# Performance work log

Hardware: AMD Instinct MI355X
Metric: run time of the kernel (lower is better)

## Reference

```python
import jax, jax.numpy as jnp
import numpy as np
from jax import lax

B, T, DIN = 512, 96, 64
H = 256          # hidden_dim
P = 2            # patch_size
L = 4            # n_layers
HEADS = 8
E = 3 * H        # encoder_dim = hidden_dim * len(scales)
NC = 100         # num_classes
EPS = 1e-5


def layernorm(x, g, b):
    m = x.mean(-1, keepdims=True)
    v = ((x - m) ** 2).mean(-1, keepdims=True)
    return (x - m) * lax.rsqrt(v + EPS) * g + b


def conv1d(x, w, b, k):
    # x: [B, C, T], w: [O, I, k]; torch padding='same' (extra pad on the right for even k)
    lo = (k - 1) // 2
    hi = (k - 1) - lo
    y = lax.conv_general_dilated(x, w, (1,), [(lo, hi)],
                                 dimension_numbers=('NCH', 'OIH', 'NCH'))
    return y + b[None, :, None]


def fourier_attn(x, Wqkv, Wo, bo):
    Bx, Tx, Ex = x.shape
    dh = Ex // HEADS
    qkv = x @ Wqkv                                   # [B,T,3E]
    q, k, v = jnp.split(qkv, 3, axis=-1)
    to_heads = lambda t: t.reshape(Bx, Tx, HEADS, dh).transpose(0, 2, 1, 3)  # [B,h,T,dh]
    q, k, v = to_heads(q), to_heads(k), to_heads(v)
    qf = jnp.fft.rfft(q, axis=-2)
    kf = jnp.fft.rfft(k, axis=-2)
    attn = jnp.sum(jnp.conj(qf) * kf, axis=-1).real * (dh ** -0.5)  # [B,h,F]
    attn = jax.nn.softmax(attn, axis=-1)
    vf = jnp.fft.rfft(v, axis=-2)                    # [B,h,F,dh]
    out = jnp.fft.irfft(attn[..., None] * vf, n=Tx, axis=-2)        # [B,h,T,dh]
    out = out.transpose(0, 2, 1, 3).reshape(Bx, Tx, Ex)
    return out @ Wo + bo


def setup_inputs() -> dict:
    key = jax.random.key(0)
    ks = iter(jax.random.split(key, 40))
    nrm = lambda shape, s=0.02: jax.random.normal(next(ks), shape, jnp.float32) * s
    z = lambda *shape: jnp.zeros(shape, jnp.float32)
    o = lambda *shape: jnp.ones(shape, jnp.float32)
    return dict(
        x=jax.random.normal(next(ks), (B, T, DIN), jnp.float32),
        W_in=nrm((DIN, H)), b_in=z(H),
        pe=nrm((1, 100, H)),
        W_shape=nrm((H, H)), b_shape=z(H),
        W_patch=nrm((P * H, H)), b_patch=z(H),
        conv_w1=nrm((H, H, 1)), conv_b1=z(H),
        conv_w2=nrm((H, H, 2)), conv_b2=z(H),
        conv_w4=nrm((H, H, 4)), conv_b4=z(H),
        ln1_g=o(L, E), ln1_b=z(L, E),
        Wqkv=nrm((L, E, 3 * E)),
        Wo=nrm((L, E, E)), bo=z(L, E),
        ln2_g=o(L, E), ln2_b=z(L, E),
        Wf1=nrm((L, E, 4 * E)), bf1=z(L, 4 * E),
        Wf2=nrm((L, 4 * E, E)), bf2=z(L, E),
        ssm_w=nrm((E, E, 3)), ssm_b=z(E),
        ssm_g=o(E), ssm_bn=z(E),
        W_out=nrm((E, NC)), b_out=z(NC),
    )


def reference(x, W_in, b_in, pe, W_shape, b_shape, W_patch, b_patch,
              conv_w1, conv_b1, conv_w2, conv_b2, conv_w4, conv_b4,
              ln1_g, ln1_b, Wqkv, Wo, bo, ln2_g, ln2_b, Wf1, bf1, Wf2, bf2,
              ssm_w, ssm_b, ssm_g, ssm_bn, W_out, b_out):
    h = x @ W_in + b_in                              # [B,T,H]
    h = h + pe[:, :h.shape[1], :]
    # shape-aware embedding: diff with prepend of first step
    sf = jnp.diff(h, axis=1, prepend=h[:, :1, :])
    h = h + sf @ W_shape + b_shape
    # patch embedding: [B,T,H] -> [B,T/P,P*H] -> [B,T/P,H]
    Bx, Tx, Dx = h.shape
    h = h.reshape(Bx, Tx // P, P * Dx) @ W_patch + b_patch
    # multiscale fourier: rfft.real then 3 same-padded convs, concat channels
    f = jnp.fft.rfft(h, axis=1).real                 # [B,F,H], F = T/P//2 + 1
    fc = f.transpose(0, 2, 1)                        # [B,H,F]
    m1 = conv1d(fc, conv_w1, conv_b1, 1).transpose(0, 2, 1)
    m2 = conv1d(fc, conv_w2, conv_b2, 2).transpose(0, 2, 1)
    m4 = conv1d(fc, conv_w4, conv_b4, 4).transpose(0, 2, 1)
    h = jnp.concatenate([m1, m2, m4], axis=-1)       # [B,F,E]
    for i in range(L):
        h = h + fourier_attn(layernorm(h, ln1_g[i], ln1_b[i]), Wqkv[i], Wo[i], bo[i])
        y = layernorm(h, ln2_g[i], ln2_b[i])
        y = jax.nn.gelu(y @ Wf1[i] + bf1[i], approximate=False) @ Wf2[i] + bf2[i]
        h = h + y
    # simple SSM: depth conv residual + layernorm
    s = conv1d(h.transpose(0, 2, 1), ssm_w, ssm_b, 3).transpose(0, 2, 1)
    h = layernorm(h + s, ssm_g, ssm_bn)
    return h.mean(axis=1) @ W_out + b_out            # [B,NC]
```

## Files before the change

kernel.cpp:

```cpp
#include <hip/hip_runtime.h>
#include <hip/hip_bf16.h>
#include <math.h>

#define Bsz 512
#define Tin 96
#define DIN 64
#define Hd  256
#define Pp  2
#define Ll  4
#define NHEAD 8
#define Ed  768
#define NCls 100
#define Tp  48
#define Ff  25
#define F2  13
#define DH  96

#define E_BIAS 1
#define E_PE   2
#define E_RES  4
#define E_ACC  8
#define E_GELU 16
#define E_OUTS 32
#define E_SPLK 64

typedef unsigned short ushortT;
typedef unsigned short ushort8 __attribute__((ext_vector_type(8)));
typedef short short8 __attribute__((ext_vector_type(8)));
typedef float f32x4 __attribute__((ext_vector_type(4)));

static __device__ __forceinline__ ushortT f2bf(float f) {
  __hip_bfloat16 h = __float2bfloat16(f);
  return *reinterpret_cast<ushortT*>(&h);
}
static __device__ __forceinline__ float bfbits2f(ushortT u) {
  unsigned int x = ((unsigned int)u) << 16;
  return __uint_as_float(x);
}
static __device__ __forceinline__ void split2(float v, ushortT& h, ushortT& l) {
  h = f2bf(v);
  l = f2bf(v - bfbits2f(h));
}

typedef const __attribute__((address_space(1))) void* gas1_t;
typedef __attribute__((address_space(3))) void* las3_t;
static __device__ __forceinline__ void gload16(const void* g, void* l) {
  __builtin_amdgcn_global_load_lds((gas1_t)g, (las3_t)l, 16, 0, 0);
}

constexpr int GBN = 128, GBK = 32;

template<int BMS, int AMODE, int ASRC, int EPI>
__global__ __launch_bounds__(256) void gemm3(
    const float* __restrict__ A,
    const ushortT* __restrict__ Ah, const ushortT* __restrict__ Al,
    const ushortT* __restrict__ Bh, const ushortT* __restrict__ Bl,
    const float* __restrict__ bias, const float* __restrict__ extra,
    float* __restrict__ C, ushortT* __restrict__ Coh, ushortT* __restrict__ Col,
    int M, int N, int K, int Ald, int Tdim, int lo, int Kin, int Cld, int coff,
    int Mt, int Nt, int mmaj, int ksn)
{
  constexpr int GBMv = BMS;
  constexpr int WMF  = GBMv / 32;
  constexpr int ARPW = GBMv / 4;
  constexpr int TPR  = 256 / GBMv;
  constexpr int EPT  = 32 / TPR;

  __shared__ __align__(16) ushortT Ash[GBMv * GBK];
  __shared__ __align__(16) ushortT Asl[GBMv * GBK];
  __shared__ __align__(16) ushortT Bsh[GBN * GBK];
  __shared__ __align__(16) ushortT Bsl[GBN * GBK];
  int tid = threadIdx.x;

  int lin = blockIdx.x;
  int G = gridDim.x;
  int r8 = lin & 7, s8 = lin >> 3;
  int q = G >> 3, rem = G & 7;
  int start = r8 * q + (r8 < rem ? r8 : rem);
  int idx = start + s8;
  int tiles = Mt * Nt;
  int ks = 0;
  if (ksn > 1) { ks = idx / tiles; idx -= ks * tiles; }
  int mt, nt;
  if (mmaj) { mt = idx / Nt; nt = idx - mt * Nt; }
  else      { nt = idx / Mt; mt = idx - nt * Mt; }
  int m0 = mt * GBMv, n0 = nt * GBN;
  int kper = K / ksn;
  int kbeg = ks * kper, kend = kbeg + kper;

  int wid = tid >> 6, lane = tid & 63;
  int wm = wid & 1, wn = wid >> 1;
  int m16 = lane & 15, quad = lane >> 4;

  f32x4 acc[WMF][4] = {};

  int gcb = (lane & 3) << 4;
  int growB = (wid << 5) + (lane >> 2);
  int scbB  = gcb ^ (((growB >> 1) & 3) << 4);
  char* ldsB = (char*)Bsh + (wid << 11);
  char* ldsb = (char*)Bsl + (wid << 11);
  size_t bo0 = ((size_t)(n0 + growB) * K) * 2 + scbB;
  size_t bo1 = bo0 + (size_t)16 * K * 2;
  int growA = wid * ARPW + (lane >> 2);
  int scbA  = gcb ^ (((growA >> 1) & 3) << 4);
  char* ldsA = (char*)Ash + wid * ARPW * 64;
  char* ldsa = (char*)Asl + wid * ARPW * 64;
  size_t ao0 = 0, ao1 = 0;
  if (ASRC == 1) {
    int ar0 = m0 + growA;  if (ar0 >= M) ar0 = M - 1;
    ao0 = ((size_t)ar0 * Ald) * 2 + scbA;
    if (ARPW == 32) {
      int ar1 = m0 + growA + 16;  if (ar1 >= M) ar1 = M - 1;
      ao1 = ((size_t)ar1 * Ald) * 2 + scbA;
    }
  }

  int srow = tid / TPR;
  int sseg = (tid % TPR) * EPT;
  int sswz = ((srow >> 1) & 3) << 3;

  int fswz = ((m16 >> 1) & 3) << 3;
  int scf  = (quad << 3) ^ fswz;

  for (int k0 = kbeg; k0 < kend; k0 += GBK) {
    size_t kb = (size_t)k0 * 2;
    gload16((const char*)Bh + bo0 + kb, ldsB);
    gload16((const char*)Bh + bo1 + kb, ldsB + 1024);
    gload16((const char*)Bl + bo0 + kb, ldsb);
    gload16((const char*)Bl + bo1 + kb, ldsb + 1024);
    if (ASRC == 1) {
      gload16((const char*)Ah + ao0 + kb, ldsA);
      gload16((const char*)Al + ao0 + kb, ldsa);
      if (ARPW == 32) {
        gload16((const char*)Ah + ao1 + kb, ldsA + 1024);
        gload16((const char*)Al + ao1 + kb, ldsa + 1024);
      }
    } else {
      int row = m0 + srow;
      if (row >= M) row = M - 1;
      float tf[EPT];
      if (AMODE == 0) {
        const float* p = A + (size_t)row * Ald + k0 + sseg;
#pragma unroll
        for (int j = 0; j < EPT; j += 4) {
          float4 v = *(const float4*)(p + j);
          tf[j] = v.x; tf[j+1] = v.y; tf[j+2] = v.z; tf[j+3] = v.w;
        }
      } else if (AMODE == 1) {
        int t = row % Tdim;
        const float* p = A + (size_t)row * Ald + k0 + sseg;
#pragma unroll
        for (int j = 0; j < EPT; j += 4) {
          float4 v = *(const float4*)(p + j);
          float4 w = (t != 0) ? *(const float4*)(p - Ald + j) : v;
          tf[j] = v.x - w.x; tf[j+1] = v.y - w.y;
          tf[j+2] = v.z - w.z; tf[j+3] = v.w - w.w;
        }
      } else {
        int kk = k0 + sseg;
        int tap = kk / Kin;
        int i0  = kk - tap * Kin;
        int bb = row / Tdim;
        int t  = row - bb * Tdim;
        int tt = t - lo + tap;
        if (tt >= 0 && tt < Tdim) {
          const float* p = A + ((size_t)bb * Tdim + tt) * Ald + i0;
#pragma unroll
          for (int j = 0; j < EPT; j += 4) {
            float4 v = *(const float4*)(p + j);
            tf[j] = v.x; tf[j+1] = v.y; tf[j+2] = v.z; tf[j+3] = v.w;
          }
        } else {
#pragma unroll
          for (int j = 0; j < EPT; j++) tf[j] = 0.0f;
        }
      }
      ushortT th[EPT], tl[EPT];
#pragma unroll
      for (int j = 0; j < EPT; j++) split2(tf[j], th[j], tl[j]);
#pragma unroll
      for (int c8 = 0; c8 < EPT / 8; c8++) {
        int st = srow * GBK + ((sseg + c8 * 8) ^ sswz);
        *(ushort8*)&Ash[st] = *(ushort8*)&th[c8 * 8];
        *(ushort8*)&Asl[st] = *(ushort8*)&tl[c8 * 8];
      }
    }
    __syncthreads();
    short8 ah[WMF], al[WMF], bh[4], bl[4];
#pragma unroll
    for (int i = 0; i < WMF; i++) {
      int ro = (wm * (WMF * 16) + i * 16 + m16) * GBK + scf;
      ah[i] = *(short8*)&Ash[ro];
      al[i] = *(short8*)&Asl[ro];
    }
#pragma unroll
    for (int j = 0; j < 4; j++) {
      int ro = (wn * 64 + j * 16 + m16) * GBK + scf;
      bh[j] = *(short8*)&Bsh[ro];
      bl[j] = *(short8*)&Bsl[ro];
    }
    __builtin_amdgcn_s_setprio(1);
#pragma unroll
    for (int i = 0; i < WMF; i++)
#pragma unroll
      for (int j = 0; j < 4; j++) {
        acc[i][j] = __builtin_amdgcn_mfma_f32_16x16x32_bf16(ah[i], bh[j], acc[i][j], 0, 0, 0);
        acc[i][j] = __builtin_amdgcn_mfma_f32_16x16x32_bf16(al[i], bh[j], acc[i][j], 0, 0, 0);
        acc[i][j] = __builtin_amdgcn_mfma_f32_16x16x32_bf16(ah[i], bl[j], acc[i][j], 0, 0, 0);
      }
    __builtin_amdgcn_s_setprio(0);
    __syncthreads();
  }

#pragma unroll
  for (int i = 0; i < WMF; i++) {
#pragma unroll
    for (int j = 0; j < 4; j++) {
      int colg = n0 + wn * 64 + j * 16 + m16;
#pragma unroll
      for (int rr = 0; rr < 4; rr++) {
        int rowg = m0 + wm * (WMF * 16) + i * 16 + quad * 4 + rr;
        if (rowg >= M) continue;
        float v = acc[i][j][rr];
        if ((EPI & E_BIAS) && ks == 0) v += bias[colg];
        if (EPI & E_PE)   v += extra[(size_t)(rowg % Tdim) * N + colg];
        if (EPI & E_RES)  v += extra[(size_t)rowg * Cld + colg];
        if (EPI & E_GELU) v = 0.5f * v * (1.0f + erff(v * 0.70710678118654752f));
        size_t off = (size_t)rowg * Cld + coff + colg;
        if (EPI & E_SPLK) {
          atomicAdd(&C[off], v);
        } else if (EPI & E_OUTS) {
          ushortT h, l; split2(v, h, l);
          Coh[off] = h; Col[off] = l;
        } else {
          if (EPI & E_ACC) v += C[off];
          C[off] = v;
        }
      }
    }
  }
}

#define GEMM3(BMS_, AM, AS, EP, KS, Asrc, AhP, AlP, BhP, BlP, biasP, extraP, CP, CohP, ColP, \
              Mv, Nv, Kv, AldV, TdimV, loV, KinV, CldV, coffV) \
  do { int Mt_ = ((Mv) + (BMS_) - 1) / (BMS_), Nt_ = (Nv) / GBN; \
       int mm_ = ((Mv) >= (Nv)) ? 1 : 0; \
       gemm3<BMS_, AM, AS, EP><<<dim3(Mt_ * Nt_ * (KS)), dim3(256), 0, stream>>>( \
           Asrc, AhP, AlP, BhP, BlP, biasP, extraP, CP, CohP, ColP, \
           Mv, Nv, Kv, AldV, TdimV, loV, KinV, CldV, coffV, Mt_, Nt_, mm_, KS); } while (0)

__global__ __launch_bounds__(256) void wcvt_t_split(
    const float* __restrict__ W, ushortT* __restrict__ Wh, ushortT* __restrict__ Wl,
    int K, int N)
{
  __shared__ float t[32][33];
  int k0 = blockIdx.y * 32, n0 = blockIdx.x * 32;
  int tx = threadIdx.x;
  int ty = threadIdx.y;
#pragma unroll
  for (int dy = 0; dy < 32; dy += 8)
    t[ty + dy][tx] = W[(size_t)(k0 + ty + dy) * N + n0 + tx];
  __syncthreads();
#pragma unroll
  for (int dy = 0; dy < 32; dy += 8) {
    float v = t[tx][ty + dy];
    ushortT h, l;
    split2(v, h, l);
    size_t off = (size_t)(n0 + ty + dy) * K + k0 + tx;
    Wh[off] = h; Wl[off] = l;
  }
}

__global__ __launch_bounds__(256) void wcvt_split(
    const float* __restrict__ W, ushortT* __restrict__ Wh, ushortT* __restrict__ Wl, int n)
{
  int gid = blockIdx.x * 256 + threadIdx.x;
  int stride = gridDim.x * 256;
  for (int i = gid; i < n; i += stride) {
    ushortT h, l;
    split2(W[i], h, l);
    Wh[i] = h; Wl[i] = l;
  }
}

__global__ __launch_bounds__(256) void wcvt_split_tm(
    const float* __restrict__ W, ushortT* __restrict__ Wh, ushortT* __restrict__ Wl,
    int O, int Kin, int NT)
{
  int n = O * Kin * NT;
  int gid = blockIdx.x * 256 + threadIdx.x;
  int stride = gridDim.x * 256;
  for (int idx = gid; idx < n; idx += stride) {
    int o = idx / (Kin * NT);
    int rr = idx - o * (Kin * NT);
    int tap = rr / Kin;
    int i = rr - tap * Kin;
    float v = W[(size_t)o * Kin * NT + (size_t)i * NT + tap];
    ushortT h, l;
    split2(v, h, l);
    Wh[idx] = h; Wl[idx] = l;
  }
}

constexpr int BM = 64, BN = 64, BK = 16, TM = 4, TN = 4;
__global__ __launch_bounds__(256) void gemm_cls(
    const float* __restrict__ A, const float* __restrict__ Bw,
    const float* __restrict__ bias, float* __restrict__ C,
    int M, int N, int K, int Ald, int Cld)
{
  __shared__ alignas(16) float As[BK][BM + 4];
  __shared__ alignas(16) float Bs[BK][BN + 4];
  int tid = threadIdx.x;
  int n0 = blockIdx.x * BN;
  int m0 = blockIdx.y * BM;
  int tx = tid & 15, ty = tid >> 4;
  float acc[TM][TN];
#pragma unroll
  for (int i = 0; i < TM; i++)
#pragma unroll
    for (int j = 0; j < TN; j++) acc[i][j] = 0.0f;
  int a_m = tid >> 2, a_k = (tid & 3) * 4;
  int b_k = tid >> 4, b_n = (tid & 15) * 4;
  for (int k0 = 0; k0 < K; k0 += BK) {
    int row = m0 + a_m;
#pragma unroll
    for (int j = 0; j < 4; j++)
      As[a_k + j][a_m] = A[(size_t)row * Ald + k0 + a_k + j];
    int kk = k0 + b_k;
#pragma unroll
    for (int j = 0; j < 4; j++) {
      int nn = n0 + b_n + j;
      Bs[b_k][b_n + j] = (nn < N) ? Bw[(size_t)kk * N + nn] : 0.0f;
    }
    __syncthreads();
#pragma unroll
    for (int k = 0; k < BK; k++) {
      float4 av = *reinterpret_cast<const float4*>(&As[k][ty * TM]);
      float4 bv = *reinterpret_cast<const float4*>(&Bs[k][tx * TN]);
      float a4[4] = {av.x, av.y, av.z, av.w};
      float b4[4] = {bv.x, bv.y, bv.z, bv.w};
#pragma unroll
      for (int i = 0; i < TM; i++)
#pragma unroll
        for (int j = 0; j < TN; j++) acc[i][j] += a4[i] * b4[j];
    }
    __syncthreads();
  }
#pragma unroll
  for (int i = 0; i < TM; i++) {
    int row = m0 + ty * TM + i;
#pragma unroll
    for (int j = 0; j < TN; j++) {
      int col = n0 + tx * TN + j;
      if (col >= N) continue;
      C[(size_t)row * Cld + col] = acc[i][j] + bias[col];
    }
  }
}

__global__ __launch_bounds__(256) void rfft48_kernel(
    const float* __restrict__ hp, float* __restrict__ f)
{
  int kf = blockIdx.x;
  int b  = blockIdx.y;
  int tid = threadIdx.x;
  __shared__ float ct[48];
  if (tid < 48) {
    int rr = (kf * tid) % 48;
    ct[tid] = cosf(6.2831853071795864f * (float)rr / 48.0f);
  }
  __syncthreads();
  const float* hb = hp + (size_t)b * Tp * Hd;
  float s = 0.0f;
  for (int t = 0; t < 48; t++) s += hb[t * Hd + tid] * ct[t];
  f[((size_t)b * Ff + kf) * Hd + tid] = s;
}

__global__ __launch_bounds__(256) void attn_fused(
    const float* __restrict__ qkv,
    ushortT* __restrict__ oh, ushortT* __restrict__ ol)
{
  int bh = blockIdx.x;
  int b = bh >> 3, h = bh & 7;
  __shared__ float qs[Ff * DH], ks[Ff * DH], vs[Ff * DH];
  __shared__ float ct[F2 * Ff], st[F2 * Ff];
  __shared__ float red[F2 * DH];
  __shared__ float sm[F2];
  __shared__ float G[Ff];
  int tid = threadIdx.x;
  const float* base = qkv + (size_t)b * Ff * (3 * Ed) + h * DH;
  for (int e = tid; e < Ff * DH; e += 256) {
    int t = e / DH, d = e - t * DH;
    size_t ro = (size_t)t * (3 * Ed) + d;
    qs[e] = base[ro];
    ks[e] = base[ro + Ed];
    vs[e] = base[ro + 2 * Ed];
  }
  for (int e = tid; e < F2 * Ff; e += 256) {
    int fq = e / Ff, t = e - fq * Ff;
    int rr = (fq * t) % Ff;
    float ang = 6.2831853071795864f * (float)rr / 25.0f;
    ct[e] = cosf(ang); st[e] = sinf(ang);
  }
  __syncthreads();
  for (int e = tid; e < F2 * DH; e += 256) {
    int fq = e / DH, d = e - fq * DH;
    float qr = 0, qi = 0, kr = 0, ki = 0;
    for (int t = 0; t < Ff; t++) {
      float c = ct[fq * Ff + t], s = st[fq * Ff + t];
      float qv = qs[t * DH + d], kv = ks[t * DH + d];
      qr += qv * c; qi += qv * s; kr += kv * c; ki += kv * s;
    }
    red[e] = qr * kr + qi * ki;
  }
  __syncthreads();
  if (tid < F2) {
    float s = 0;
    for (int d = 0; d < DH; d++) s += red[tid * DH + d];
    sm[tid] = s * 0.10206207261596575f;
  }
  __syncthreads();
  if (tid == 0) {
    float mx = sm[0];
    for (int f = 1; f < F2; f++) mx = fmaxf(mx, sm[f]);
    float den = 0;
    for (int f = 0; f < F2; f++) { float e2 = expf(sm[f] - mx); sm[f] = e2; den += e2; }
    float inv = 1.0f / den;
    for (int f = 0; f < F2; f++)
      sm[f] *= inv * ((f == 0) ? (1.0f / 25.0f) : (2.0f / 25.0f));
  }
  __syncthreads();
  if (tid < Ff) {
    float g = 0;
    for (int f = 0; f < F2; f++) g += sm[f] * ct[f * Ff + tid];
    G[tid] = g;
  }
  __syncthreads();
  size_t ob = ((size_t)b * Ff) * Ed + h * DH;
  for (int e = tid; e < Ff * DH; e += 256) {
    int t = e / DH, d = e - t * DH;
    float o = 0;
    int dd = t;
    for (int tp = 0; tp < Ff; tp++) {
      o += G[dd] * vs[tp * DH + d];
      dd--; if (dd < 0) dd += Ff;
    }
    ushortT hh, ll;
    split2(o, hh, ll);
    size_t off = ob + (size_t)t * Ed + d;
    oh[off] = hh; ol[off] = ll;
  }
}

static __device__ __forceinline__ float wave_sum(float s) {
#pragma unroll
  for (int o = 32; o > 0; o >>= 1) s += __shfl_xor(s, o);
  return s;
}

__global__ __launch_bounds__(256) void ln_split(
    const float* __restrict__ x, const float* __restrict__ g,
    const float* __restrict__ bb, ushortT* __restrict__ yh, ushortT* __restrict__ yl)
{
  int row = blockIdx.x;
  int tid = threadIdx.x;
  int wid = tid >> 6, lane = tid & 63;
  const float* xr = x + (size_t)row * Ed;
  float v0 = xr[tid], v1 = xr[tid + 256], v2 = xr[tid + 512];
  __shared__ float wsum[4], wsq[4];
  float s = wave_sum(v0 + v1 + v2);
  if (lane == 0) wsum[wid] = s;
  __syncthreads();
  float m = (wsum[0] + wsum[1] + wsum[2] + wsum[3]) * (1.0f / 768.0f);
  float d0 = v0 - m, d1 = v1 - m, d2 = v2 - m;
  float q = wave_sum(d0 * d0 + d1 * d1 + d2 * d2);
  if (lane == 0) wsq[wid] = q;
  __syncthreads();
  float inv = rsqrtf((wsq[0] + wsq[1] + wsq[2] + wsq[3]) * (1.0f / 768.0f) + 1e-5f);
  size_t basei = (size_t)row * Ed;
  float o0 = d0 * inv * g[tid] + bb[tid];
  float o1 = d1 * inv * g[tid + 256] + bb[tid + 256];
  float o2 = d2 * inv * g[tid + 512] + bb[tid + 512];
  ushortT h, l;
  split2(o0, h, l); yh[basei + tid] = h;       yl[basei + tid] = l;
  split2(o1, h, l); yh[basei + tid + 256] = h; yl[basei + tid + 256] = l;
  split2(o2, h, l); yh[basei + tid + 512] = h; yl[basei + tid + 512] = l;
}

__global__ __launch_bounds__(256) void ln_f32(
    const float* __restrict__ x, const float* __restrict__ g,
    const float* __restrict__ bb, float* __restrict__ y)
{
  int row = blockIdx.x;
  int tid = threadIdx.x;
  int wid = tid >> 6, lane = tid & 63;
  const float* xr = x + (size_t)row * Ed;
  float v0 = xr[tid], v1 = xr[tid + 256], v2 = xr[tid + 512];
  __shared__ float wsum[4], wsq[4];
  float s = wave_sum(v0 + v1 + v2);
  if (lane == 0) wsum[wid] = s;
  __syncthreads();
  float m = (wsum[0] + wsum[1] + wsum[2] + wsum[3]) * (1.0f / 768.0f);
  float d0 = v0 - m, d1 = v1 - m, d2 = v2 - m;
  float q = wave_sum(d0 * d0 + d1 * d1 + d2 * d2);
  if (lane == 0) wsq[wid] = q;
  __syncthreads();
  float inv = rsqrtf((wsq[0] + wsq[1] + wsq[2] + wsq[3]) * (1.0f / 768.0f) + 1e-5f);
  float* yr = y + (size_t)row * Ed;
  yr[tid]       = d0 * inv * g[tid]       + bb[tid];
  yr[tid + 256] = d1 * inv * g[tid + 256] + bb[tid + 256];
  yr[tid + 512] = d2 * inv * g[tid + 512] + bb[tid + 512];
}

__global__ __launch_bounds__(256) void mean_kernel(
    const float* __restrict__ x, float* __restrict__ y)
{
  int b = blockIdx.x;
  int tid = threadIdx.x;
  for (int c = tid; c < Ed; c += 256) {
    float s = 0;
    for (int t = 0; t < Ff; t++) s += x[((size_t)b * Ff + t) * Ed + c];
    y[(size_t)b * Ed + c] = s * (1.0f / 25.0f);
  }
}

extern "C" void kernel_launch(void* const* d_in, const int* in_sizes, int n_in,
                              void* d_out, int out_size, void* d_ws, size_t ws_size,
                              hipStream_t stream)
{
  const float* x       = (const float*)d_in[0];
  const float* W_in    = (const float*)d_in[1];
  const float* b_in    = (const float*)d_in[2];
  const float* pe      = (const float*)d_in[3];
  const float* W_shape = (const float*)d_in[4];
  const float* b_shape = (const float*)d_in[5];
  const float* W_patch = (const float*)d_in[6];
  const float* b_patch = (const float*)d_in[7];
  const float* conv_w1 = (const float*)d_in[8];
  const float* conv_b1 = (const float*)d_in[9];
  const float* conv_w2 = (const float*)d_in[10];
  const float* conv_b2 = (const float*)d_in[11];
  const float* conv_w4 = (const float*)d_in[12];
  const float* conv_b4 = (const float*)d_in[13];
  const float* ln1_g   = (const float*)d_in[14];
  const float* ln1_b   = (const float*)d_in[15];
  const float* Wqkv    = (const float*)d_in[16];
  const float* Wo      = (const float*)d_in[17];
  const float* bo      = (const float*)d_in[18];
  const float* ln2_g   = (const float*)d_in[19];
  const float* ln2_b   = (const float*)d_in[20];
  const float* Wf1     = (const float*)d_in[21];
  const float* bf1     = (const float*)d_in[22];
  const float* Wf2     = (const float*)d_in[23];
  const float* bf2     = (const float*)d_in[24];
  const float* ssm_w   = (const float*)d_in[25];
  const float* ssm_b   = (const float*)d_in[26];
  const float* ssm_g   = (const float*)d_in[27];
  const float* ssm_bn  = (const float*)d_in[28];
  const float* W_out   = (const float*)d_in[29];
  const float* b_out   = (const float*)d_in[30];
  float* out = (float*)d_out;

  float* hbuf = (float*)d_ws;
  ushortT* Ahp = (ushortT*)(hbuf + 9830400);
  ushortT* Alp = Ahp + 9830400;
  float* pool = (float*)(Alp + 9830400);

  dim3 blk(256);
  dim3 wblk(32, 8);
  const int Mf = Bsz * Ff;
  const ushortT* NUS = nullptr;
  const float* NF = nullptr;
  ushortT* NU = nullptr;

  ushortT* p0w = (ushortT*)(pool + 6291456);
  ushortT* WinH = p0w + 0;        ushortT* WinL = p0w + 16384;
  ushortT* WshH = p0w + 32768;    ushortT* WshL = p0w + 98304;
  ushortT* WpaH = p0w + 163840;   ushortT* WpaL = p0w + 294912;
  ushortT* c1H  = p0w + 425984;   ushortT* c1L  = p0w + 491520;
  ushortT* c2H  = p0w + 557056;   ushortT* c2L  = p0w + 688128;
  ushortT* c4H  = p0w + 819200;   ushortT* c4L  = p0w + 1081344;
  wcvt_t_split<<<dim3(Hd / 32, DIN / 32), wblk, 0, stream>>>(W_in, WinH, WinL, DIN, Hd);
  wcvt_t_split<<<dim3(Hd / 32, Hd / 32), wblk, 0, stream>>>(W_shape, WshH, WshL, Hd, Hd);
  wcvt_t_split<<<dim3(Hd / 32, (Pp * Hd) / 32), wblk, 0, stream>>>(W_patch, WpaH, WpaL, Pp * Hd, Hd);
  wcvt_split<<<64, blk, 0, stream>>>(conv_w1, c1H, c1L, Hd * Hd);
  wcvt_split_tm<<<128, blk, 0, stream>>>(conv_w2, c2H, c2L, Hd, Hd, 2);
  wcvt_split_tm<<<256, blk, 0, stream>>>(conv_w4, c4H, c4L, Hd, Hd, 4);

  float* s0  = (float*)Ahp;
  float* s1f = (float*)Ahp + 6291456;
  float* s1  = pool;
  for (int c = 0; c < 2; c++) {
    const int NB = 256;
    const int M96 = NB * Tin;
    const int Mpch = NB * Tp;
    const float* xc = x + (size_t)c * NB * Tin * DIN;

    GEMM3(64, 0, 0, E_BIAS | E_PE, 1, xc, NUS, NUS, WinH, WinL, b_in, pe, s0, NU, NU,
          M96, Hd, DIN, DIN, Tin, 0, 0, Hd, 0);
    GEMM3(64, 1, 0, E_BIAS | E_RES, 1, s0, NUS, NUS, WshH, WshL, b_shape, s0, s1, NU, NU,
          M96, Hd, Hd, Hd, Tin, 0, 0, Hd, 0);
    GEMM3(64, 0, 0, E_BIAS, 1, s1, NUS, NUS, WpaH, WpaL, b_patch, NF, s0, NU, NU,
          Mpch, Hd, Pp * Hd, Pp * Hd, 0, 0, 0, Hd, 0);
    rfft48_kernel<<<dim3(Ff, NB), blk, 0, stream>>>(s0, s1f + (size_t)c * NB * Ff * Hd);
  }
  GEMM3(64, 0, 0, E_BIAS, 1, s1f, NUS, NUS, c1H, c1L, conv_b1, NF, hbuf, NU, NU,
        Mf, Hd, Hd, Hd, Ff, 0, 0, Ed, 0);
  GEMM3(64, 2, 0, E_BIAS, 1, s1f, NUS, NUS, c2H, c2L, conv_b2, NF, hbuf, NU, NU,
        Mf, Hd, Hd * 2, Hd, Ff, 0, Hd, Ed, Hd);
  GEMM3(64, 2, 0, E_BIAS, 1, s1f, NUS, NUS, c4H, c4L, conv_b4, NF, hbuf, NU, NU,
        Mf, Hd, Hd * 4, Hd, Ff, 1, Hd, Ed, 2 * Hd);

  float* qkvbuf = pool;
  ushortT* lwA = (ushortT*)(pool + 7372800);
  ushortT* qkH = lwA + 0;        ushortT* qkL = lwA + 1769472;
  ushortT* woH = lwA + 3538944;  ushortT* woL = lwA + 4128768;
  ushortT* Ch2 = (ushortT*)pool;
  ushortT* Cl2 = Ch2 + 6291456;
  ushortT* lwB = (ushortT*)(pool + 6291456);
  ushortT* f1H = lwB + 0;        ushortT* f1L = lwB + 2359296;
  ushortT* f2H = lwB + 4718592;  ushortT* f2L = lwB + 7077888;

  const int NBA = 128;
  const int Mca = NBA * Ff;

  for (int l = 0; l < Ll; l++) {
    const float* Wqkv_l = Wqkv + (size_t)l * Ed * (3 * Ed);
    const float* Wo_l   = Wo   + (size_t)l * Ed * Ed;
    const float* bo_l   = bo   + (size_t)l * Ed;
    const float* Wf1_l  = Wf1  + (size_t)l * Ed * (4 * Ed);
    const float* bf1_l  = bf1  + (size_t)l * (4 * Ed);
    const float* Wf2_l  = Wf2  + (size_t)l * (4 * Ed) * Ed;
    const float* bf2_l  = bf2  + (size_t)l * Ed;

    wcvt_t_split<<<dim3((3 * Ed) / 32, Ed / 32), wblk, 0, stream>>>(Wqkv_l, qkH, qkL, Ed, 3 * Ed);
    wcvt_t_split<<<dim3(Ed / 32, Ed / 32), wblk, 0, stream>>>(Wo_l, woH, woL, Ed, Ed);

    ln_split<<<Mf, blk, 0, stream>>>(hbuf, ln1_g + (size_t)l * Ed, ln1_b + (size_t)l * Ed, Ahp, Alp);

    for (int c = 0; c < 4; c++) {
      ushortT* ah = Ahp + (size_t)c * Mca * Ed;
      ushortT* al = Alp + (size_t)c * Mca * Ed;
      GEMM3(64, 0, 1, 0, 1, NF, ah, al, qkH, qkL, NF, NF, qkvbuf, NU, NU,
            Mca, 3 * Ed, Ed, Ed, 0, 0, 0, 3 * Ed, 0);
      attn_fused<<<NBA * NHEAD, blk, 0, stream>>>(qkvbuf, ah, al);
    }
    GEMM3(128, 0, 1, E_BIAS | E_SPLK, 2, NF, Ahp, Alp, woH, woL, bo_l, NF, hbuf, NU, NU,
          Mf, Ed, Ed, Ed, 0, 0, 0, Ed, 0);

    wcvt_t_split<<<dim3((4 * Ed) / 32, Ed / 32), wblk, 0, stream>>>(Wf1_l, f1H, f1L, Ed, 4 * Ed);
    wcvt_t_split<<<dim3(Ed / 32, (4 * Ed) / 32), wblk, 0, stream>>>(Wf2_l, f2H, f2L, 4 * Ed, Ed);

    ln_split<<<Mf, blk, 0, stream>>>(hbuf, ln2_g + (size_t)l * Ed, ln2_b + (size_t)l * Ed, Ahp, Alp);

    for (int row0 = 0; row0 < Mf; row0 += 2048) {
      int rows = (Mf - row0 < 2048) ? (Mf - row0) : 2048;
      GEMM3(64, 0, 1, E_BIAS | E_GELU | E_OUTS, 1, NF,
            Ahp + (size_t)row0 * Ed, Alp + (size_t)row0 * Ed, f1H, f1L, bf1_l, NF,
            (float*)nullptr, Ch2, Cl2, rows, 4 * Ed, Ed, Ed, 0, 0, 0, 4 * Ed, 0);
      GEMM3(64, 0, 1, E_BIAS | E_SPLK, 4, NF, Ch2, Cl2, f2H, f2L, bf2_l, NF,
            hbuf + (size_t)row0 * Ed, NU, NU, rows, Ed, 4 * Ed, 4 * Ed, 0, 0, 0, Ed, 0);
    }
  }

  ushortT* ssH = (ushortT*)pool; ushortT* ssL = ssH + 1769472;
  wcvt_split_tm<<<512, blk, 0, stream>>>(ssm_w, ssH, ssL, Ed, Ed, 3);
  float* S = (float*)Ahp;
  GEMM3(128, 2, 0, E_BIAS | E_RES, 1, hbuf, NUS, NUS, ssH, ssL, ssm_b, hbuf, S, NU, NU,
        Mf, Ed, Ed * 3, Ed, Ff, 1, Ed, Ed, 0);

  float* L = pool;
  ln_f32<<<Mf, blk, 0, stream>>>(S, ssm_g, ssm_bn, L);
  float* mout = (float*)Ahp;
  mean_kernel<<<Bsz, blk, 0, stream>>>(L, mout);
  gemm_cls<<<dim3(2, Bsz / BM), blk, 0, stream>>>(
      mout, W_out, b_out, out, Bsz, NCls, Ed, Ed, NCls);
}
```

Baseline: 5.478 ms.

## Add 64x64x64 GEMM tile variant for bf16-split transformer GEMMs

Adds a new gemm3 path with a 64x64 output tile and BK=64, using an XOR-swizzled LDS layout and 16x16x32 bf16 MFMAs for the hi/lo split products. The QKV, Wo, FFN1 and FFN2 GEMMs switch to it, and Wo moves from a 128-row tile to 64 rows. The smaller tiles give more blocks and halve the number of K-loop barriers per element of K. In exchange each block reuses less data and moves more global traffic per FLOP.

```diff
diff --git a/kernel.cpp b/kernel.cpp
--- a/kernel.cpp
+++ b/kernel.cpp
@@ -48,9 +48,9 @@
   __builtin_amdgcn_global_load_lds((gas1_t)g, (las3_t)l, 16, 0, 0);
 }
 
-constexpr int GBN = 128, GBK = 32;
-
-template<int BMS, int AMODE, int ASRC, int EPI>
+constexpr int GBK = 32;
+
+template<int BMS, int GBKT, int AMODE, int ASRC, int EPI>
 __global__ __launch_bounds__(256) void gemm3(
     const float* __restrict__ A,
     const ushortT* __restrict__ Ah, const ushortT* __restrict__ Al,
@@ -61,15 +61,16 @@
     int Mt, int Nt, int mmaj, int ksn)
 {
   constexpr int GBMv = BMS;
+  constexpr int GBNv = (GBKT == 64) ? 64 : 128;
   constexpr int WMF  = GBMv / 32;
   constexpr int ARPW = GBMv / 4;
   constexpr int TPR  = 256 / GBMv;
   constexpr int EPT  = 32 / TPR;
 
-  __shared__ __align__(16) ushortT Ash[GBMv * GBK];
-  __shared__ __align__(16) ushortT Asl[GBMv * GBK];
-  __shared__ __align__(16) ushortT Bsh[GBN * GBK];
-  __shared__ __align__(16) ushortT Bsl[GBN * GBK];
+  __shared__ __align__(16) ushortT Ash[GBMv * GBKT];
+  __shared__ __align__(16) ushortT Asl[GBMv * GBKT];
+  __shared__ __align__(16) ushortT Bsh[GBNv * GBKT];
+  __shared__ __align__(16) ushortT Bsl[GBNv * GBKT];
   int tid = threadIdx.x;
 
   int lin = blockIdx.x;
@@ -84,7 +85,7 @@
   int mt, nt;
   if (mmaj) { mt = idx / Nt; nt = idx - mt * Nt; }
   else      { nt = idx / Mt; mt = idx - nt * Mt; }
-  int m0 = mt * GBMv, n0 = nt * GBN;
+  int m0 = mt * GBMv, n0 = nt * GBNv;
   int kper = K / ksn;
   int kbeg = ks * kper, kend = kbeg + kper;
 
@@ -92,6 +93,90 @@
   int wm = wid & 1, wn = wid >> 1;
   int m16 = lane & 15, quad = lane >> 4;
 
+  if constexpr (GBKT == 64) {
+    f32x4 acc[2][2] = {};
+    int rowg = lane >> 3;
+    int colb = (lane & 7) << 4;
+    int scb  = colb ^ (rowg << 4);
+    int gr0  = (wid << 4) + rowg;
+    int a0 = m0 + gr0;      if (a0 >= M) a0 = M - 1;
+    int a1 = m0 + gr0 + 8;  if (a1 >= M) a1 = M - 1;
+    size_t ao0 = ((size_t)a0 * Ald) * 2 + scb;
+    size_t ao1 = ((size_t)a1 * Ald) * 2 + scb;
+    size_t bo0 = ((size_t)(n0 + gr0) * K) * 2 + scb;
+    size_t bo1 = bo0 + (size_t)8 * K * 2;
+    char* lA = (char*)Ash + (wid << 11);
+    char* la = (char*)Asl + (wid << 11);
+    char* lB = (char*)Bsh + (wid << 11);
+    char* lb = (char*)Bsl + (wid << 11);
+    int fswz = (m16 & 7) << 4;
+
+    for (int k0 = kbeg; k0 < kend; k0 += 64) {
+      size_t kb = (size_t)k0 * 2;
+      gload16((const char*)Bh + bo0 + kb, lB);
+      gload16((const char*)Bh + bo1 + kb, lB + 1024);
+      gload16((const char*)Bl + bo0 + kb, lb);
+      gload16((const char*)Bl + bo1 + kb, lb + 1024);
+      gload16((const char*)Ah + ao0 + kb, lA);
+      gload16((const char*)Ah + ao1 + kb, lA + 1024);
+      gload16((const char*)Al + ao0 + kb, la);
+      gload16((const char*)Al + ao1 + kb, la + 1024);
+      __syncthreads();
+      short8 ah[2][2], al2[2][2], bh[2][2], bl[2][2];
+#pragma unroll
+      for (int kk = 0; kk < 2; kk++) {
+        int cb = (kk << 6) + (quad << 4);
+#pragma unroll
+        for (int i = 0; i < 2; i++) {
+          int ra = ((wm << 5) + (i << 4) + m16) * 128 + (cb ^ fswz);
+          ah[kk][i]  = *(short8*)((char*)Ash + ra);
+          al2[kk][i] = *(short8*)((char*)Asl + ra);
+          int rb = ((wn << 5) + (i << 4) + m16) * 128 + (cb ^ fswz);
+          bh[kk][i] = *(short8*)((char*)Bsh + rb);
+          bl[kk][i] = *(short8*)((char*)Bsl + rb);
+        }
+      }
+      __builtin_amdgcn_s_setprio(1);
+#pragma unroll
+      for (int kk = 0; kk < 2; kk++)
+#pragma unroll
+        for (int i = 0; i < 2; i++)
+#pragma unroll
+          for (int j = 0; j < 2; j++) {
+            acc[i][j] = __builtin_amdgcn_mfma_f32_16x16x32_bf16(ah[kk][i], bh[kk][j], acc[i][j], 0, 0, 0);
+            acc[i][j] = __builtin_amdgcn_mfma_f32_16x16x32_bf16(al2[kk][i], bh[kk][j], acc[i][j], 0, 0, 0);
+            acc[i][j] = __builtin_amdgcn_mfma_f32_16x16x32_bf16(ah[kk][i], bl[kk][j], acc[i][j], 0, 0, 0);
+          }
+      __builtin_amdgcn_s_setprio(0);
+      __syncthreads();
+    }
+#pragma unroll
+    for (int i = 0; i < 2; i++) {
+#pragma unroll
+      for (int j = 0; j < 2; j++) {
+        int colg = n0 + (wn << 5) + (j << 4) + m16;
+#pragma unroll
+        for (int rr = 0; rr < 4; rr++) {
+          int rowg2 = m0 + (wm << 5) + (i << 4) + (quad << 2) + rr;
+          if (rowg2 >= M) continue;
+          float v = acc[i][j][rr];
+          if ((EPI & E_BIAS) && ks == 0) v += bias[colg];
+          if (EPI & E_GELU) v = 0.5f * v * (1.0f + erff(v * 0.70710678118654752f));
+          size_t off = (size_t)rowg2 * Cld + coff + colg;
+          if (EPI & E_SPLK) {
+            atomicAdd(&C[off], v);
+          } else if (EPI & E_OUTS) {
+            ushortT h, l; split2(v, h, l);
+            Coh[off] = h; Col[off] = l;
+          } else {
+            if (EPI & E_ACC) v += C[off];
+            C[off] = v;
+          }
+        }
+      }
+    }
+    return;
+  } else {
   f32x4 acc[WMF][4] = {};
 
   int gcb = (lane & 3) << 4;
@@ -239,13 +324,15 @@
       }
     }
   }
-}
-
-#define GEMM3(BMS_, AM, AS, EP, KS, Asrc, AhP, AlP, BhP, BlP, biasP, extraP, CP, CohP, ColP, \
+  }
+}
+
+#define GEMM3(BMS_, GBK_, AM, AS, EP, KS, Asrc, AhP, AlP, BhP, BlP, biasP, extraP, CP, CohP, ColP, \
               Mv, Nv, Kv, AldV, TdimV, loV, KinV, CldV, coffV) \
-  do { int Mt_ = ((Mv) + (BMS_) - 1) / (BMS_), Nt_ = (Nv) / GBN; \
+  do { int Mt_ = ((Mv) + (BMS_) - 1) / (BMS_); \
+       int Nt_ = (Nv) / (((GBK_) == 64) ? 64 : 128); \
        int mm_ = ((Mv) >= (Nv)) ? 1 : 0; \
-       gemm3<BMS_, AM, AS, EP><<<dim3(Mt_ * Nt_ * (KS)), dim3(256), 0, stream>>>( \
+       gemm3<BMS_, GBK_, AM, AS, EP><<<dim3(Mt_ * Nt_ * (KS)), dim3(256), 0, stream>>>( \
            Asrc, AhP, AlP, BhP, BlP, biasP, extraP, CP, CohP, ColP, \
            Mv, Nv, Kv, AldV, TdimV, loV, KinV, CldV, coffV, Mt_, Nt_, mm_, KS); } while (0)
 
@@ -596,19 +683,19 @@
     const int Mpch = NB * Tp;
     const float* xc = x + (size_t)c * NB * Tin * DIN;
 
-    GEMM3(64, 0, 0, E_BIAS | E_PE, 1, xc, NUS, NUS, WinH, WinL, b_in, pe, s0, NU, NU,
+    GEMM3(64, 32, 0, 0, E_BIAS | E_PE, 1, xc, NUS, NUS, WinH, WinL, b_in, pe, s0, NU, NU,
           M96, Hd, DIN, DIN, Tin, 0, 0, Hd, 0);
-    GEMM3(64, 1, 0, E_BIAS | E_RES, 1, s0, NUS, NUS, WshH, WshL, b_shape, s0, s1, NU, NU,
+    GEMM3(64, 32, 1, 0, E_BIAS | E_RES, 1, s0, NUS, NUS, WshH, WshL, b_shape, s0, s1, NU, NU,
           M96, Hd, Hd, Hd, Tin, 0, 0, Hd, 0);
-    GEMM3(64, 0, 0, E_BIAS, 1, s1, NUS, NUS, WpaH, WpaL, b_patch, NF, s0, NU, NU,
+    GEMM3(64, 32, 0, 0, E_BIAS, 1, s1, NUS, NUS, WpaH, WpaL, b_patch, NF, s0, NU, NU,
           Mpch, Hd, Pp * Hd, Pp * Hd, 0, 0, 0, Hd, 0);
     rfft48_kernel<<<dim3(Ff, NB), blk, 0, stream>>>(s0, s1f + (size_t)c * NB * Ff * Hd);
   }
-  GEMM3(64, 0, 0, E_BIAS, 1, s1f, NUS, NUS, c1H, c1L, conv_b1, NF, hbuf, NU, NU,
+  GEMM3(64, 32, 0, 0, E_BIAS, 1, s1f, NUS, NUS, c1H, c1L, conv_b1, NF, hbuf, NU, NU,
         Mf, Hd, Hd, Hd, Ff, 0, 0, Ed, 0);
-  GEMM3(64, 2, 0, E_BIAS, 1, s1f, NUS, NUS, c2H, c2L, conv_b2, NF, hbuf, NU, NU,
+  GEMM3(64, 32, 2, 0, E_BIAS, 1, s1f, NUS, NUS, c2H, c2L, conv_b2, NF, hbuf, NU, NU,
         Mf, Hd, Hd * 2, Hd, Ff, 0, Hd, Ed, Hd);
-  GEMM3(64, 2, 0, E_BIAS, 1, s1f, NUS, NUS, c4H, c4L, conv_b4, NF, hbuf, NU, NU,
+  GEMM3(64, 32, 2, 0, E_BIAS, 1, s1f, NUS, NUS, c4H, c4L, conv_b4, NF, hbuf, NU, NU,
         Mf, Hd, Hd * 4, Hd, Ff, 1, Hd, Ed, 2 * Hd);
 
   float* qkvbuf = pool;
@@ -641,11 +728,11 @@
     for (int c = 0; c < 4; c++) {
       ushortT* ah = Ahp + (size_t)c * Mca * Ed;
       ushortT* al = Alp + (size_t)c * Mca * Ed;
-      GEMM3(64, 0, 1, 0, 1, NF, ah, al, qkH, qkL, NF, NF, qkvbuf, NU, NU,
+      GEMM3(64, 64, 0, 1, 0, 1, NF, ah, al, qkH, qkL, NF, NF, qkvbuf, NU, NU,
             Mca, 3 * Ed, Ed, Ed, 0, 0, 0, 3 * Ed, 0);
       attn_fused<<<NBA * NHEAD, blk, 0, stream>>>(qkvbuf, ah, al);
     }
-    GEMM3(128, 0, 1, E_BIAS | E_SPLK, 2, NF, Ahp, Alp, woH, woL, bo_l, NF, hbuf, NU, NU,
+    GEMM3(64, 64, 0, 1, E_BIAS | E_SPLK, 2, NF, Ahp, Alp, woH, woL, bo_l, NF, hbuf, NU, NU,
           Mf, Ed, Ed, Ed, 0, 0, 0, Ed, 0);
 
     wcvt_t_split<<<dim3((4 * Ed) / 32, Ed / 32), wblk, 0, stream>>>(Wf1_l, f1H, f1L, Ed, 4 * Ed);
@@ -655,10 +742,10 @@
 
     for (int row0 = 0; row0 < Mf; row0 += 2048) {
       int rows = (Mf - row0 < 2048) ? (Mf - row0) : 2048;
-      GEMM3(64, 0, 1, E_BIAS | E_GELU | E_OUTS, 1, NF,
+      GEMM3(64, 64, 0, 1, E_BIAS | E_GELU | E_OUTS, 1, NF,
             Ahp + (size_t)row0 * Ed, Alp + (size_t)row0 * Ed, f1H, f1L, bf1_l, NF,
             (float*)nullptr, Ch2, Cl2, rows, 4 * Ed, Ed, Ed, 0, 0, 0, 4 * Ed, 0);
-      GEMM3(64, 0, 1, E_BIAS | E_SPLK, 4, NF, Ch2, Cl2, f2H, f2L, bf2_l, NF,
+      GEMM3(64, 64, 0, 1, E_BIAS | E_SPLK, 4, NF, Ch2, Cl2, f2H, f2L, bf2_l, NF,
             hbuf + (size_t)row0 * Ed, NU, NU, rows, Ed, 4 * Ed, 4 * Ed, 0, 0, 0, Ed, 0);
     }
   }
@@ -666,7 +753,7 @@
   ushortT* ssH = (ushortT*)pool; ushortT* ssL = ssH + 1769472;
   wcvt_split_tm<<<512, blk, 0, stream>>>(ssm_w, ssH, ssL, Ed, Ed, 3);
   float* S = (float*)Ahp;
-  GEMM3(128, 2, 0, E_BIAS | E_RES, 1, hbuf, NUS, NUS, ssH, ssL, ssm_b, hbuf, S, NU, NU,
+  GEMM3(128, 32, 2, 0, E_BIAS | E_RES, 1, hbuf, NUS, NUS, ssH, ssL, ssm_b, hbuf, S, NU, NU,
         Mf, Ed, Ed * 3, Ed, Ff, 1, Ed, Ed, 0);
 
   float* L = pool;
```

Result: faster. 5.076 ms (-7.3%).
